# Kernel tuning notes

Measured on AMD Instinct MI355X. Metric: run time of the kernel, lower is better.

The kernel has to match this reference:

```python
import jax, jax.numpy as jnp
import numpy as np

D_MODEL = 1024
N_HEADS = 16
HEAD_DIM = D_MODEL // N_HEADS


def setup_inputs() -> dict:
    key = jax.random.key(0)
    ks = jax.random.split(key, 6)
    B, S = 2, 2048
    scale = 1.0 / np.sqrt(D_MODEL)
    x = jax.random.normal(ks[0], (B, S, D_MODEL), dtype=jnp.float32)
    Wq = jax.random.normal(ks[1], (D_MODEL, D_MODEL), dtype=jnp.float32) * scale
    Wk = jax.random.normal(ks[2], (D_MODEL, D_MODEL), dtype=jnp.float32) * scale
    Wv = jax.random.normal(ks[3], (D_MODEL, D_MODEL), dtype=jnp.float32) * scale
    Wo = jax.random.normal(ks[4], (D_MODEL, D_MODEL), dtype=jnp.float32) * scale
    bo = jax.random.normal(ks[5], (D_MODEL,), dtype=jnp.float32) * 0.02
    return {"x": x, "Wq": Wq, "Wk": Wk, "Wv": Wv, "Wo": Wo, "bo": bo}


def reference(x, Wq, Wk, Wv, Wo, bo):
    B, S, _ = x.shape
    H, hd = N_HEADS, HEAD_DIM
    # qkv projections (no bias, qkv_bias=False)
    q = (x @ Wq).reshape(B, S, H, hd).transpose(0, 2, 1, 3)  # [B,H,S,hd]
    k = (x @ Wk).reshape(B, S, H, hd).transpose(0, 2, 1, 3)
    v = (x @ Wv).reshape(B, S, H, hd).transpose(0, 2, 1, 3)
    scores = jnp.einsum('bhqd,bhkd->bhqk', q, k)  # [B,H,S,S]
    causal = jnp.tril(jnp.ones((S, S), dtype=bool))  # True = keep
    scores = jnp.where(causal, scores, -jnp.inf)
    weights = jax.nn.softmax(scores / np.sqrt(hd), axis=-1)
    # dropout p=0.0 -> identity
    ctx = jnp.einsum('bhqk,bhkd->bhqd', weights, v)  # [B,H,S,hd]
    ctx = ctx.transpose(0, 2, 1, 3).reshape(B, S, H * hd)
    return ctx @ Wo + bo
```

## Files before the change

kernel.cpp:

```cpp
#include <hip/hip_runtime.h>
#include <hip/hip_bf16.h>
#include <stdint.h>

#define SEQ    2048
#define BATCH  2
#define DMODEL 1024
#define NHEADS 16
#define HDIM   64
#define MROWS  (BATCH*SEQ)

typedef __attribute__((ext_vector_type(8))) short bf16x8;
typedef __attribute__((ext_vector_type(4))) short bf16x4;
typedef __attribute__((ext_vector_type(4))) float f32x4;

__device__ inline void global_to_lds16(const void* g, void* l) {
  __builtin_amdgcn_global_load_lds(
      (const __attribute__((address_space(1))) uint32_t*)g,
      (__attribute__((address_space(3))) uint32_t*)l, 16, 0, 0);
}

__device__ inline unsigned short f2bf_bits(float f) {
  __hip_bfloat16 h = __float2bfloat16(f);
  return *(unsigned short*)&h;
}

__global__ void cvt_x(const float* __restrict__ x, __hip_bfloat16* __restrict__ xb) {
  int i = (blockIdx.x * 256 + threadIdx.x) * 4;
  float4 v = *(const float4*)(x + i);
  ushort4 o;
  o.x = f2bf_bits(v.x); o.y = f2bf_bits(v.y);
  o.z = f2bf_bits(v.z); o.w = f2bf_bits(v.w);
  *(ushort4*)(xb + i) = o;
}

__global__ void trans_w(const float* __restrict__ Wq, const float* __restrict__ Wk,
                        const float* __restrict__ Wv, const float* __restrict__ Wo,
                        __hip_bfloat16* __restrict__ Wqkv_t, __hip_bfloat16* __restrict__ Wo_t) {
  __shared__ float tile[32][33];
  int z = blockIdx.z;
  const float* W = (z == 0) ? Wq : (z == 1) ? Wk : (z == 2) ? Wv : Wo;
  __hip_bfloat16* dst = (z < 3) ? (Wqkv_t + (size_t)z * 1024 * 1024) : Wo_t;
  int k0 = blockIdx.x * 32, n0 = blockIdx.y * 32;
  int tx = threadIdx.x & 31, ty = threadIdx.x >> 5;
#pragma unroll
  for (int r = 0; r < 4; r++)
    tile[ty + r * 8][tx] = W[(size_t)(k0 + ty + r * 8) * 1024 + n0 + tx];
  __syncthreads();
#pragma unroll
  for (int r = 0; r < 4; r++)
    dst[(size_t)(n0 + ty + r * 8) * 1024 + k0 + tx] = __float2bfloat16(tile[tx][ty + r * 8]);
}

__global__ void trans_v(const __hip_bfloat16* __restrict__ QKV, __hip_bfloat16* __restrict__ Vt) {
  __shared__ __hip_bfloat16 tile[64][72];
  int bh = blockIdx.y;
  int b = bh >> 4, h = bh & 15;
  int s0 = blockIdx.x * 64;
  int t = threadIdx.x;
  int r = t >> 2, cg = (t & 3) * 16;
  const __hip_bfloat16* src = QKV + ((size_t)(b * SEQ + s0 + r)) * 3072 + 2048 + h * 64 + cg;
  *(uint4*)&tile[r][cg]     = *(const uint4*)src;
  *(uint4*)&tile[r][cg + 8] = *(const uint4*)(src + 8);
  __syncthreads();
  unsigned short tmp[16];
#pragma unroll
  for (int i = 0; i < 16; i++) tmp[i] = *(const unsigned short*)&tile[cg + i][r];
  __hip_bfloat16* dst = Vt + ((size_t)bh * 64 + r) * 2048 + s0 + cg;
  *(uint4*)dst       = *(const uint4*)&tmp[0];
  *(uint4*)(dst + 8) = *(const uint4*)&tmp[8];
}

template <int TN, bool OUT_BF16, int MINW>
__global__ __launch_bounds__(256, MINW)
void gemm_kernel(const __hip_bfloat16* __restrict__ A, const __hip_bfloat16* __restrict__ Bt,
                 void* __restrict__ C, const float* __restrict__ bias, int ldc) {
  __shared__ __hip_bfloat16 Asl[128 * 64];
  __shared__ __hip_bfloat16 Bsl[TN * 64];

  const int t = threadIdx.x;
  const int lane = t & 63;
  const int w = t >> 6;
  constexpr int MI = (TN == 128) ? 4 : 2;
  const int wrow = (TN == 128) ? (w >> 1) * 64 : w * 32;
  const int wcol = (TN == 128) ? (w & 1) * 64 : 0;
  const int m0 = blockIdx.y * 128;
  const int n0 = blockIdx.x * TN;

  f32x4 acc[MI][4];
#pragma unroll
  for (int i = 0; i < MI; i++)
#pragma unroll
    for (int j = 0; j < 4; j++) acc[i][j] = (f32x4){0.f, 0.f, 0.f, 0.f};

  const int srow = lane >> 3;
  const int sjc = (lane & 7) ^ srow;
  const int fm = lane & 15;
  const int g4 = lane >> 4;

  for (int k0 = 0; k0 < 1024; k0 += 64) {
#pragma unroll
    for (int i = 0; i < 4; i++) {
      int seg = i * 4 + w;
      int r = seg * 8 + srow;
      global_to_lds16(A + (size_t)(m0 + r) * 1024 + k0 + sjc * 8,
                      (void*)(Asl + seg * 512 + lane * 8));
    }
#pragma unroll
    for (int i = 0; i < TN / 32; i++) {
      int seg = i * 4 + w;
      int r = seg * 8 + srow;
      global_to_lds16(Bt + (size_t)(n0 + r) * 1024 + k0 + sjc * 8,
                      (void*)(Bsl + seg * 512 + lane * 8));
    }
    __syncthreads();
#pragma unroll
    for (int kb = 0; kb < 2; kb++) {
      bf16x8 af[MI], bfr[4];
#pragma unroll
      for (int mi = 0; mi < MI; mi++) {
        int row = wrow + mi * 16 + fm;
        af[mi] = *(const bf16x8*)(Asl + row * 64 + (((kb * 4 + g4) ^ (row & 7)) << 3));
      }
#pragma unroll
      for (int ni = 0; ni < 4; ni++) {
        int row = wcol + ni * 16 + fm;
        bfr[ni] = *(const bf16x8*)(Bsl + row * 64 + (((kb * 4 + g4) ^ (row & 7)) << 3));
      }
#pragma unroll
      for (int mi = 0; mi < MI; mi++)
#pragma unroll
        for (int ni = 0; ni < 4; ni++)
          acc[mi][ni] = __builtin_amdgcn_mfma_f32_16x16x32_bf16(af[mi], bfr[ni], acc[mi][ni], 0, 0, 0);
    }
    __syncthreads();
  }

#pragma unroll
  for (int mi = 0; mi < MI; mi++) {
    int mb = m0 + wrow + mi * 16 + g4 * 4;
#pragma unroll
    for (int ni = 0; ni < 4; ni++) {
      int n = n0 + wcol + ni * 16 + fm;
      float bv = OUT_BF16 ? 0.f : bias[n];
#pragma unroll
      for (int r = 0; r < 4; r++) {
        if (OUT_BF16)
          ((__hip_bfloat16*)C)[(size_t)(mb + r) * ldc + n] = __float2bfloat16(acc[mi][ni][r]);
        else
          ((float*)C)[(size_t)(mb + r) * ldc + n] = acc[mi][ni][r] + bv;
      }
    }
  }
}

__global__ __launch_bounds__(256, 3)
void attn_kernel(const __hip_bfloat16* __restrict__ QKV,
                 const __hip_bfloat16* __restrict__ Vt,
                 __hip_bfloat16* __restrict__ ctx) {
  __shared__ __hip_bfloat16 Klds[2][64 * 64];
  __shared__ __hip_bfloat16 Vlds[2][64 * 64];

  const int t = threadIdx.x;
  const int lane = t & 63;
  const int w = t >> 6;
  const int jb = blockIdx.x;
  const int qtab[2] = { jb, 31 - jb };
  const int bh = blockIdx.y;
  const int b = bh >> 4, h = bh & 15;
  const int fm = lane & 15;
  const int g4 = lane >> 4;
  const int fk = g4 * 8;
  const size_t rowb = (size_t)b * SEQ;
  const float c = 0.18033688011112042f;

  const int krr = lane >> 3;
  const int kjc = (lane & 7) ^ krr;

  bf16x8 qf[2][2];
#pragma unroll
  for (int hh = 0; hh < 2; hh++) {
    const __hip_bfloat16* qp = QKV + (rowb + qtab[hh] * 64 + w * 16 + fm) * 3072 + h * 64 + fk;
    bf16x8 r0 = *(const bf16x8*)qp;
    bf16x8 r1 = *(const bf16x8*)(qp + 32);
#pragma unroll
    for (int i = 0; i < 8; i++) {
      float f0 = __uint_as_float(((unsigned)(unsigned short)r0[i]) << 16) * c;
      float f1 = __uint_as_float(((unsigned)(unsigned short)r1[i]) << 16) * c;
      r0[i] = (short)f2bf_bits(f0);
      r1[i] = (short)f2bf_bits(f1);
    }
    qf[hh][0] = r0; qf[hh][1] = r1;
  }

  bf16x4 ones4;
#pragma unroll
  for (int i = 0; i < 4; i++) ones4[i] = (short)0x3F80;

  f32x4 acc[2][4];
  f32x4 lacc[2];
#pragma unroll
  for (int hh = 0; hh < 2; hh++) {
    lacc[hh] = (f32x4){0.f, 0.f, 0.f, 0.f};
#pragma unroll
    for (int d = 0; d < 4; d++) acc[hh][d] = (f32x4){0.f, 0.f, 0.f, 0.f};
  }

  auto stage = [&](int kts, int bufi) {
    const int kt0 = kts * 64;
#pragma unroll
    for (int i = 0; i < 2; i++) {
      int seg = w + i * 4;
      int r = seg * 8 + krr;
      global_to_lds16(QKV + (rowb + kt0 + r) * 3072 + 1024 + h * 64 + kjc * 8,
                      (void*)(&Klds[bufi][0] + seg * 512 + lane * 8));
      global_to_lds16(Vt + ((size_t)bh * 64 + r) * 2048 + kt0 + kjc * 8,
                      (void*)(&Vlds[bufi][0] + seg * 512 + lane * 8));
    }
  };

  const int lastt = qtab[1];
  stage(0, 0);
  for (int kts = 0; kts <= lastt; ++kts) {
    __syncthreads();
    if (kts < lastt) stage(kts + 1, (kts + 1) & 1);
    const __hip_bfloat16* Kb = &Klds[kts & 1][0];
    const __hip_bfloat16* Vb = &Vlds[kts & 1][0];
    const bool act0 = (kts <= qtab[0]);

    bf16x4 vf[4][4];
#pragma unroll
    for (int dd = 0; dd < 4; dd++)
#pragma unroll
      for (int ns = 0; ns < 4; ns++)
        vf[dd][ns] = *(const bf16x4*)(Vb + (dd * 16 + fm) * 64 +
                                      (((2 * ns + (g4 >> 1)) ^ (fm & 7)) << 3) + (g4 & 1) * 4);

    f32x4 st1[4], st0[4];
#pragma unroll
    for (int ns = 0; ns < 4; ns++) {
      st1[ns] = (f32x4){0.f, 0.f, 0.f, 0.f};
      st0[ns] = (f32x4){0.f, 0.f, 0.f, 0.f};
    }
#pragma unroll
    for (int kk = 0; kk < 2; kk++) {
      bf16x8 kf[4];
#pragma unroll
      for (int ns = 0; ns < 4; ns++)
        kf[ns] = *(const bf16x8*)(Kb + (ns * 16 + fm) * 64 + (((kk * 4 + g4) ^ (fm & 7)) << 3));
#pragma unroll
      for (int ns = 0; ns < 4; ns++)
        st1[ns] = __builtin_amdgcn_mfma_f32_16x16x32_bf16(kf[ns], qf[1][kk], st1[ns], 0, 0, 0);
      if (act0)
#pragma unroll
        for (int ns = 0; ns < 4; ns++)
          st0[ns] = __builtin_amdgcn_mfma_f32_16x16x32_bf16(kf[ns], qf[0][kk], st0[ns], 0, 0, 0);
    }

    auto half = [&](const f32x4 (&st)[4], int hh) {
      const bool diag = (kts == qtab[hh]);
#pragma unroll
      for (int ns = 0; ns < 4; ns++) {
        float e[4];
#pragma unroll
        for (int r = 0; r < 4; r++) {
          float p = __builtin_amdgcn_exp2f(st[ns][r]);
          if (diag) {
            int ktl = ns * 16 + g4 * 4 + r;
            p = (ktl > w * 16 + fm) ? 0.f : p;
          }
          e[r] = p;
        }
        unsigned lo = __builtin_amdgcn_perm(__builtin_bit_cast(unsigned, e[1]),
                                            __builtin_bit_cast(unsigned, e[0]), 0x07060302u);
        unsigned hi = __builtin_amdgcn_perm(__builtin_bit_cast(unsigned, e[3]),
                                            __builtin_bit_cast(unsigned, e[2]), 0x07060302u);
        uint2 pp; pp.x = lo; pp.y = hi;
        bf16x4 pf = __builtin_bit_cast(bf16x4, pp);
        lacc[hh] = __builtin_amdgcn_mfma_f32_16x16x16bf16_1k(pf, ones4, lacc[hh], 0, 0, 0);
#pragma unroll
        for (int dd = 0; dd < 4; dd++)
          acc[hh][dd] = __builtin_amdgcn_mfma_f32_16x16x16bf16_1k(pf, vf[dd][ns], acc[hh][dd], 0, 0, 0);
      }
    };
    half(st1, 1);
    if (act0) half(st0, 0);
  }

#pragma unroll
  for (int hh = 0; hh < 2; hh++) {
    float rl[4];
#pragma unroll
    for (int r = 0; r < 4; r++) rl[r] = __builtin_amdgcn_rcpf(lacc[hh][r]);
#pragma unroll
    for (int dd = 0; dd < 4; dd++)
#pragma unroll
      for (int r = 0; r < 4; r++) {
        int q = qtab[hh] * 64 + w * 16 + g4 * 4 + r;
        ctx[(rowb + q) * 1024 + h * 64 + dd * 16 + fm] =
            __float2bfloat16(acc[hh][dd][r] * rl[r]);
      }
  }
}

extern "C" void kernel_launch(void* const* d_in, const int* in_sizes, int n_in,
                              void* d_out, int out_size, void* d_ws, size_t ws_size,
                              hipStream_t stream) {
  const float* x  = (const float*)d_in[0];
  const float* Wq = (const float*)d_in[1];
  const float* Wk = (const float*)d_in[2];
  const float* Wv = (const float*)d_in[3];
  const float* Wo = (const float*)d_in[4];
  const float* bo = (const float*)d_in[5];
  float* out = (float*)d_out;

  char* ws = (char*)d_ws;
  __hip_bfloat16* xb     = (__hip_bfloat16*)(ws);
  __hip_bfloat16* Wqkv_t = (__hip_bfloat16*)(ws + (8ull  << 20));
  __hip_bfloat16* Wo_t   = (__hip_bfloat16*)(ws + (14ull << 20));
  __hip_bfloat16* QKV    = (__hip_bfloat16*)(ws + (16ull << 20));
  __hip_bfloat16* ctxb   = (__hip_bfloat16*)(ws + (40ull << 20));
  __hip_bfloat16* Vt     = xb;

  cvt_x<<<dim3(MROWS * DMODEL / (256 * 4)), dim3(256), 0, stream>>>(x, xb);
  trans_w<<<dim3(32, 32, 4), dim3(256), 0, stream>>>(Wq, Wk, Wv, Wo, Wqkv_t, Wo_t);
  gemm_kernel<128, true, 3><<<dim3(24, 32), dim3(256), 0, stream>>>(xb, Wqkv_t, (void*)QKV, nullptr, 3072);
  trans_v<<<dim3(32, 32), dim3(256), 0, stream>>>(QKV, Vt);
  attn_kernel<<<dim3(16, 32), dim3(256), 0, stream>>>(QKV, Vt, ctxb);
  gemm_kernel<64, false, 2><<<dim3(16, 32), dim3(256), 0, stream>>>(ctxb, Wo_t, (void*)out, bo, 1024);
}
```

Baseline: 190.0 us.

## Stage 128-key tiles per barrier in attention and alternate block order by head

The attention kernel now loads K/V tiles of 128 keys per double-buffered stage instead of 64. Each tile is processed as two 64-key subchunks, which halves the number of __syncthreads and global-to-LDS stage rounds. The V layout and swizzle are widened to 128 columns, and the query-block index is reversed for half the heads so heavy and light causal work interleaves across the grid. The cost is doubled LDS use (64KB), which is why the occupancy hint drops from 3 to 2 blocks.

```diff
diff --git a/kernel.cpp b/kernel.cpp
--- a/kernel.cpp
+++ b/kernel.cpp
@@ -153,19 +153,19 @@
   }
 }
 
-__global__ __launch_bounds__(256, 3)
+__global__ __launch_bounds__(256, 2)
 void attn_kernel(const __hip_bfloat16* __restrict__ QKV,
                  const __hip_bfloat16* __restrict__ Vt,
                  __hip_bfloat16* __restrict__ ctx) {
-  __shared__ __hip_bfloat16 Klds[2][64 * 64];
-  __shared__ __hip_bfloat16 Vlds[2][64 * 64];
+  __shared__ __hip_bfloat16 Klds[2][128 * 64];
+  __shared__ __hip_bfloat16 Vlds[2][64 * 128];
 
   const int t = threadIdx.x;
   const int lane = t & 63;
   const int w = t >> 6;
-  const int jb = blockIdx.x;
+  const int bh = blockIdx.y;
+  const int jb = (int)blockIdx.x ^ ((bh & 16) ? 15 : 0);
   const int qtab[2] = { jb, 31 - jb };
-  const int bh = blockIdx.y;
   const int b = bh >> 4, h = bh & 15;
   const int fm = lane & 15;
   const int g4 = lane >> 4;
@@ -175,6 +175,7 @@
 
   const int krr = lane >> 3;
   const int kjc = (lane & 7) ^ krr;
+  const int vrr = lane >> 4;
 
   bf16x8 qf[2][2];
 #pragma unroll
@@ -205,85 +206,98 @@
     for (int d = 0; d < 4; d++) acc[hh][d] = (f32x4){0.f, 0.f, 0.f, 0.f};
   }
 
-  auto stage = [&](int kts, int bufi) {
-    const int kt0 = kts * 64;
-#pragma unroll
-    for (int i = 0; i < 2; i++) {
-      int seg = w + i * 4;
-      int r = seg * 8 + krr;
-      global_to_lds16(QKV + (rowb + kt0 + r) * 3072 + 1024 + h * 64 + kjc * 8,
+  auto stage = [&](int pt, int bufi) {
+    const int kt0 = pt * 128;
+#pragma unroll
+    for (int i = 0; i < 4; i++) {
+      int seg = i * 4 + w;
+      int kr = seg * 8 + krr;
+      global_to_lds16(QKV + (rowb + kt0 + kr) * 3072 + 1024 + h * 64 + kjc * 8,
                       (void*)(&Klds[bufi][0] + seg * 512 + lane * 8));
-      global_to_lds16(Vt + ((size_t)bh * 64 + r) * 2048 + kt0 + kjc * 8,
+      int vd = seg * 4 + vrr;
+      int vjc = (lane & 15) ^ ((seg & 1) * 4 + vrr);
+      global_to_lds16(Vt + ((size_t)bh * 64 + vd) * 2048 + kt0 + vjc * 8,
                       (void*)(&Vlds[bufi][0] + seg * 512 + lane * 8));
     }
   };
 
   const int lastt = qtab[1];
+  const int lastp = lastt >> 1;
   stage(0, 0);
-  for (int kts = 0; kts <= lastt; ++kts) {
+  for (int pt = 0; pt <= lastp; ++pt) {
     __syncthreads();
-    if (kts < lastt) stage(kts + 1, (kts + 1) & 1);
-    const __hip_bfloat16* Kb = &Klds[kts & 1][0];
-    const __hip_bfloat16* Vb = &Vlds[kts & 1][0];
-    const bool act0 = (kts <= qtab[0]);
-
-    bf16x4 vf[4][4];
-#pragma unroll
-    for (int dd = 0; dd < 4; dd++)
-#pragma unroll
-      for (int ns = 0; ns < 4; ns++)
-        vf[dd][ns] = *(const bf16x4*)(Vb + (dd * 16 + fm) * 64 +
-                                      (((2 * ns + (g4 >> 1)) ^ (fm & 7)) << 3) + (g4 & 1) * 4);
-
-    f32x4 st1[4], st0[4];
-#pragma unroll
-    for (int ns = 0; ns < 4; ns++) {
-      st1[ns] = (f32x4){0.f, 0.f, 0.f, 0.f};
-      st0[ns] = (f32x4){0.f, 0.f, 0.f, 0.f};
-    }
-#pragma unroll
-    for (int kk = 0; kk < 2; kk++) {
-      bf16x8 kf[4];
-#pragma unroll
-      for (int ns = 0; ns < 4; ns++)
-        kf[ns] = *(const bf16x8*)(Kb + (ns * 16 + fm) * 64 + (((kk * 4 + g4) ^ (fm & 7)) << 3));
-#pragma unroll
-      for (int ns = 0; ns < 4; ns++)
-        st1[ns] = __builtin_amdgcn_mfma_f32_16x16x32_bf16(kf[ns], qf[1][kk], st1[ns], 0, 0, 0);
-      if (act0)
+    if (pt < lastp) stage(pt + 1, (pt + 1) & 1);
+    const __hip_bfloat16* Kb = &Klds[pt & 1][0];
+    const __hip_bfloat16* Vb = &Vlds[pt & 1][0];
+
+#pragma unroll
+    for (int sc = 0; sc < 2; sc++) {
+      const int kts = pt * 2 + sc;
+      if (kts > lastt) break;
+      const bool act0 = (kts <= qtab[0]);
+
+      f32x4 st1[4], st0[4];
+#pragma unroll
+      for (int ns = 0; ns < 4; ns++) {
+        st1[ns] = (f32x4){0.f, 0.f, 0.f, 0.f};
+        st0[ns] = (f32x4){0.f, 0.f, 0.f, 0.f};
+      }
+#pragma unroll
+      for (int kk = 0; kk < 2; kk++) {
+        bf16x8 kf[4];
+#pragma unroll
+        for (int ns = 0; ns < 4; ns++) {
+          int row = sc * 64 + ns * 16 + fm;
+          kf[ns] = *(const bf16x8*)(Kb + row * 64 + (((kk * 4 + g4) ^ (fm & 7)) << 3));
+        }
 #pragma unroll
         for (int ns = 0; ns < 4; ns++)
-          st0[ns] = __builtin_amdgcn_mfma_f32_16x16x32_bf16(kf[ns], qf[0][kk], st0[ns], 0, 0, 0);
-    }
-
-    auto half = [&](const f32x4 (&st)[4], int hh) {
-      const bool diag = (kts == qtab[hh]);
-#pragma unroll
-      for (int ns = 0; ns < 4; ns++) {
-        float e[4];
-#pragma unroll
-        for (int r = 0; r < 4; r++) {
-          float p = __builtin_amdgcn_exp2f(st[ns][r]);
-          if (diag) {
-            int ktl = ns * 16 + g4 * 4 + r;
-            p = (ktl > w * 16 + fm) ? 0.f : p;
+          st1[ns] = __builtin_amdgcn_mfma_f32_16x16x32_bf16(kf[ns], qf[1][kk], st1[ns], 0, 0, 0);
+        if (act0)
+#pragma unroll
+          for (int ns = 0; ns < 4; ns++)
+            st0[ns] = __builtin_amdgcn_mfma_f32_16x16x32_bf16(kf[ns], qf[0][kk], st0[ns], 0, 0, 0);
+      }
+
+      bf16x4 vf[4][4];
+#pragma unroll
+      for (int dd = 0; dd < 4; dd++)
+#pragma unroll
+        for (int ns = 0; ns < 4; ns++) {
+          int ch = sc * 8 + ns * 2 + (g4 >> 1);
+          vf[dd][ns] = *(const bf16x4*)(Vb + (dd * 16 + fm) * 128 +
+                                        ((ch ^ (fm & 7)) << 3) + (g4 & 1) * 4);
+        }
+
+      auto half = [&](const f32x4 (&st)[4], int hh) {
+        const bool diag = (kts == qtab[hh]);
+#pragma unroll
+        for (int ns = 0; ns < 4; ns++) {
+          float e[4];
+#pragma unroll
+          for (int r = 0; r < 4; r++) {
+            float p = __builtin_amdgcn_exp2f(st[ns][r]);
+            if (diag) {
+              int ktl = ns * 16 + g4 * 4 + r;
+              p = (ktl > w * 16 + fm) ? 0.f : p;
+            }
+            e[r] = p;
           }
-          e[r] = p;
+          unsigned lo = __builtin_amdgcn_perm(__builtin_bit_cast(unsigned, e[1]),
+                                              __builtin_bit_cast(unsigned, e[0]), 0x07060302u);
+          unsigned hi = __builtin_amdgcn_perm(__builtin_bit_cast(unsigned, e[3]),
+                                              __builtin_bit_cast(unsigned, e[2]), 0x07060302u);
+          uint2 pp; pp.x = lo; pp.y = hi;
+          bf16x4 pf = __builtin_bit_cast(bf16x4, pp);
+          lacc[hh] = __builtin_amdgcn_mfma_f32_16x16x16bf16_1k(pf, ones4, lacc[hh], 0, 0, 0);
+#pragma unroll
+          for (int dd = 0; dd < 4; dd++)
+            acc[hh][dd] = __builtin_amdgcn_mfma_f32_16x16x16bf16_1k(pf, vf[dd][ns], acc[hh][dd], 0, 0, 0);
         }
-        unsigned lo = __builtin_amdgcn_perm(__builtin_bit_cast(unsigned, e[1]),
-                                            __builtin_bit_cast(unsigned, e[0]), 0x07060302u);
-        unsigned hi = __builtin_amdgcn_perm(__builtin_bit_cast(unsigned, e[3]),
-                                            __builtin_bit_cast(unsigned, e[2]), 0x07060302u);
-        uint2 pp; pp.x = lo; pp.y = hi;
-        bf16x4 pf = __builtin_bit_cast(bf16x4, pp);
-        lacc[hh] = __builtin_amdgcn_mfma_f32_16x16x16bf16_1k(pf, ones4, lacc[hh], 0, 0, 0);
-#pragma unroll
-        for (int dd = 0; dd < 4; dd++)
-          acc[hh][dd] = __builtin_amdgcn_mfma_f32_16x16x16bf16_1k(pf, vf[dd][ns], acc[hh][dd], 0, 0, 0);
-      }
-    };
-    half(st1, 1);
-    if (act0) half(st0, 0);
+      };
+      half(st1, 1);
+      if (act0) half(st0, 0);
+    }
   }
 
 #pragma unroll
```

New measurement: 175.6 us. -7.6%, faster.
